# Optimization experiments

Measured on AMD Instinct MI355X. Metric: run time of the kernel, lower is better.

Reference implementation:

```python
import jax, jax.numpy as jnp
import numpy as np

B, IN, OUT, LAT = 8192, 256, 256, 128

def setup_inputs() -> dict:
    key = jax.random.key(0)
    ks = jax.random.split(key, 6)
    s = 0.05
    return {
        "x": jax.random.normal(ks[0], (B, IN), dtype=jnp.float32),
        "latent": jax.random.normal(ks[1], (B, LAT), dtype=jnp.float32),
        "Ww": jax.random.normal(ks[2], (LAT, IN * OUT), dtype=jnp.float32) * s,
        "bw": jax.random.normal(ks[3], (IN * OUT,), dtype=jnp.float32) * s,
        "Wb": jax.random.normal(ks[4], (LAT, OUT), dtype=jnp.float32) * s,
        "bb": jax.random.normal(ks[5], (OUT,), dtype=jnp.float32) * s,
    }

def reference(x, latent, Ww, bw, Wb, bb):
    lead = x.shape[:-1]
    x2 = x.reshape(-1, x.shape[-1])            # [B, in]
    l2 = latent.reshape(-1, latent.shape[-1])  # [B, lat]
    # per-sample weight: [B, in, out]
    weight = (l2 @ Ww + bw).reshape(-1, IN, OUT)
    # per-sample bias: [B, out]
    bias = l2 @ Wb + bb
    out = jnp.einsum('bi,bio->bo', x2, weight) + bias
    return out.reshape(*lead, OUT)
```

## Files before the change

kernel.cpp:

```cpp
#include <hip/hip_runtime.h>
#include <cstdint>
#include <cstddef>

#define BATCH  8192
#define IN_N   256
#define OUT_N  256
#define LAT_N  128
#define SLABS  129
#define KT     (SLABS * IN_N)
#define KT16   (KT / 16)
#define SPLITK 4

typedef _Float16 h8 __attribute__((ext_vector_type(8)));
typedef _Float16 h4 __attribute__((ext_vector_type(4)));
typedef _Float16 h2 __attribute__((ext_vector_type(2)));
typedef float    f16v __attribute__((ext_vector_type(16)));
typedef float    f4v  __attribute__((ext_vector_type(4)));

#define WS_BP    0
#define WS_XH    16908288
#define WS_LT    21102592
#define WS_PARTS 23216128

#define PR_T1   516
#define PR_L1   580
#define PR_X1   1604
#define PR_O1   1608
#define PR_B1   2632
__global__ void k_prep(const float* __restrict__ Ww, const float* __restrict__ bw,
                       const float* __restrict__ x,  const float* __restrict__ latent,
                       const float* __restrict__ Wb, const float* __restrict__ bb,
                       _Float16* __restrict__ Bp, _Float16* __restrict__ Xh,
                       _Float16* __restrict__ LT, float* __restrict__ part0) {
    __shared__ _Float16 smemh[16512];
    const int bid = blockIdx.x;
    const int t   = threadIdx.x;

    if (bid < PR_T1) {
        _Float16* tile = smemh;
        const int k0 = bid * 64;
#pragma unroll
        for (int j = 0; j < 16; ++j) {
            int idx = j * 256 + t;
            int row = idx >> 6, col = (idx & 63) * 4;
            int k = k0 + row;
            const float* src = (k < LAT_N * IN_N)
                             ? Ww + (size_t)k * 256 + col
                             : bw + (size_t)(k - LAT_N * IN_N) * 256 + col;
            float4 v = *(const float4*)src;
            h4 o;
            o[0] = (_Float16)v.x; o[1] = (_Float16)v.y;
            o[2] = (_Float16)v.z; o[3] = (_Float16)v.w;
            *(h4*)(tile + row * 256 + col) = o;
        }
        __syncthreads();
        const int tl = t & 31;
#pragma unroll
        for (int j = 0; j < 4; ++j) {
            int stid = j * 8 + (t >> 5);
            int kt_l = stid >> 3, nt = stid & 7;
            int kt16 = bid * 4 + kt_l;
            _Float16* dst = Bp + ((size_t)(nt * KT16 + kt16) * 64) * 8;
#pragma unroll
            for (int kh = 0; kh < 2; ++kh) {
                h8 v;
#pragma unroll
                for (int h = 0; h < 8; ++h)
                    v[h] = tile[(kt_l * 16 + kh * 8 + h) * 256 + nt * 32 + tl];
                *(h8*)(dst + (size_t)(kh * 32 + tl) * 8) = v;
            }
        }
    } else if (bid < PR_L1) {
        _Float16* t2 = smemh;
        const int b0 = (bid - PR_T1) * 128;
#pragma unroll
        for (int j = 0; j < 16; ++j) {
            int idx = j * 256 + t;
            int b = idx >> 5, l = (idx & 31) * 4;
            float4 v = *(const float4*)(latent + (size_t)(b0 + b) * 128 + l);
            t2[(l + 0) * 129 + b] = (_Float16)v.x;
            t2[(l + 1) * 129 + b] = (_Float16)v.y;
            t2[(l + 2) * 129 + b] = (_Float16)v.z;
            t2[(l + 3) * 129 + b] = (_Float16)v.w;
        }
        __syncthreads();
#pragma unroll
        for (int j = 0; j < 32; ++j) {
            int idx = j * 256 + t;
            int l = idx >> 6, bb = (idx & 63) * 2;
            h2 w;
            w[0] = t2[l * 129 + bb];
            w[1] = t2[l * 129 + bb + 1];
            *(h2*)(LT + (size_t)l * BATCH + b0 + bb) = w;
        }
    } else if (bid < PR_X1) {
        const int cb = bid - PR_L1;
        int i = (cb * 256 + t) * 8;
        float4 v0 = *(const float4*)(x + i);
        float4 v1 = *(const float4*)(x + i + 4);
        h8 o;
        o[0] = (_Float16)v0.x; o[1] = (_Float16)v0.y;
        o[2] = (_Float16)v0.z; o[3] = (_Float16)v0.w;
        o[4] = (_Float16)v1.x; o[5] = (_Float16)v1.y;
        o[6] = (_Float16)v1.z; o[7] = (_Float16)v1.w;
        *(h8*)(Xh + i) = o;
    } else if (bid < PR_O1) {
        const int ob = bid - PR_X1;
        int base = ob * 2048 + t * 8;
        h8 o;
#pragma unroll
        for (int h = 0; h < 8; ++h) o[h] = (_Float16)1.0f;
        *(h8*)(LT + (size_t)LAT_N * BATCH + base) = o;
    } else {
        float* lat = (float*)smemh;
        const int b0 = (bid - PR_O1) * 8;
#pragma unroll
        for (int j = 0; j < 4; ++j) {
            int idx = t + 256 * j;
            int rr = idx >> 7, l = idx & 127;
            lat[rr * 128 + l] = latent[(size_t)(b0 + rr) * 128 + l];
        }
        __syncthreads();
        const int o = t;
        float acc[8];
        float bbv = bb[o];
#pragma unroll
        for (int rr = 0; rr < 8; ++rr) acc[rr] = bbv;
        for (int l = 0; l < 128; ++l) {
            float w = Wb[l * 256 + o];
#pragma unroll
            for (int rr = 0; rr < 8; ++rr) acc[rr] += lat[rr * 128 + l] * w;
        }
#pragma unroll
        for (int rr = 0; rr < 8; ++rr) part0[(size_t)(b0 + rr) * 256 + o] = acc[rr];
    }
}

__global__ __launch_bounds__(256, 2) void k_gemm(const _Float16* __restrict__ Bp,
                                                 const _Float16* __restrict__ Xh,
                                                 const _Float16* __restrict__ LT,
                                                 float* __restrict__ parts) {
    __shared__ _Float16 Xs[64 * 256];

    const int bid   = blockIdx.x;
    const int m_blk = bid >> 2;
    const int ks    = bid & 3;
    const int m0    = m_blk * 64;
    const int slab0 = (ks == 0) ? 0 : 33 + 32 * (ks - 1);
    const int nslab = (ks == 0) ? 33 : 32;

    const int tid = threadIdx.x, wid = tid >> 6, lane = tid & 63;
    const int l32 = lane & 31, khalf = lane >> 5;

    for (int j = 0; j < 8; ++j) {
        int G = j * 256 + tid;
        int m = G >> 5, gp = G & 31;
        int g = gp ^ (m & 7);
        h8 v = *(const h8*)(Xh + (size_t)(m0 + m) * IN_N + g * 8);
        *(h8*)(Xs + m * IN_N + gp * 8) = v;
    }
    __syncthreads();

    int mrow[2], m7[2], pbase[2], m6[2];
#pragma unroll
    for (int t = 0; t < 2; ++t) {
        mrow[t]  = t * 32 + l32;
        m7[t]    = mrow[t] & 7;
        m6[t]    = m7[t] & 6;
        pbase[t] = mrow[t] * IN_N + (khalf ^ (m7[t] & 1)) * 8;
    }

    const _Float16* ltp = LT + (size_t)slab0 * BATCH + m0;
    _Float16 s_cur[2], s_nxt[2];
#pragma unroll
    for (int t = 0; t < 2; ++t) s_cur[t] = ltp[mrow[t]];

    const _Float16* bp0 = Bp + ((size_t)((wid * 2 + 0) * KT16 + slab0 * 16) * 64 + lane) * 8;
    const _Float16* bp1 = Bp + ((size_t)((wid * 2 + 1) * KT16 + slab0 * 16) * 64 + lane) * 8;

    f16v acc[2][2];
#pragma unroll
    for (int t = 0; t < 2; ++t)
#pragma unroll
        for (int u = 0; u < 2; ++u)
#pragma unroll
            for (int r = 0; r < 16; ++r) acc[t][u][r] = 0.0f;

    for (int sl = 0; sl < nslab; ++sl) {
        if (sl) {
#pragma unroll
            for (int t = 0; t < 2; ++t) s_cur[t] = s_nxt[t];
        }
        if (sl + 1 < nslab) {
            const _Float16* p = ltp + (size_t)(sl + 1) * BATCH;
#pragma unroll
            for (int t = 0; t < 2; ++t) s_nxt[t] = p[mrow[t]];
        }
        h8 s8[2];
#pragma unroll
        for (int t = 0; t < 2; ++t) {
            _Float16 s = s_cur[t];
            s8[t][0]=s; s8[t][1]=s; s8[t][2]=s; s8[t][3]=s;
            s8[t][4]=s; s8[t][5]=s; s8[t][6]=s; s8[t][7]=s;
        }
        const _Float16* b0p = bp0 + (size_t)sl * (16 * 512);
        const _Float16* b1p = bp1 + (size_t)sl * (16 * 512);
#pragma unroll
        for (int ks16 = 0; ks16 < 16; ++ks16) {
            h8 b0 = *(const h8*)(b0p + ks16 * 512);
            h8 b1 = *(const h8*)(b1p + ks16 * 512);
            h8 a[2];
#pragma unroll
            for (int t = 0; t < 2; ++t) {
                int off = pbase[t] + ((ks16 * 2) ^ m6[t]) * 8;
                h8 xv = *(const h8*)(Xs + off);
                a[t] = xv * s8[t];
            }
#pragma unroll
            for (int t = 0; t < 2; ++t) {
                acc[t][0] = __builtin_amdgcn_mfma_f32_32x32x16_f16(a[t], b0, acc[t][0], 0, 0, 0);
                acc[t][1] = __builtin_amdgcn_mfma_f32_32x32x16_f16(a[t], b1, acc[t][1], 0, 0, 0);
            }
        }
    }

    float* dst = parts + (size_t)ks * ((size_t)BATCH * OUT_N);
#pragma unroll
    for (int t = 0; t < 2; ++t) {
        int rowb = m0 + t * 32;
#pragma unroll
        for (int u = 0; u < 2; ++u) {
            int col = wid * 64 + u * 32 + l32;
#pragma unroll
            for (int r = 0; r < 16; ++r) {
                int row = rowb + (r & 3) + 8 * (r >> 2) + 4 * khalf;
                size_t off = (size_t)row * OUT_N + col;
                float v = acc[t][u][r];
                if (ks == 0) dst[off] += v;
                else         dst[off] = v;
            }
        }
    }
}

__global__ void k_reduce(const float* __restrict__ parts, float* __restrict__ out) {
    int i = (blockIdx.x * 256 + threadIdx.x) * 4;
    f4v s = *(const f4v*)(parts + i);
    s += *(const f4v*)(parts + 2097152 + i);
    s += *(const f4v*)(parts + 2 * 2097152 + i);
    s += *(const f4v*)(parts + 3 * 2097152 + i);
    *(f4v*)(out + i) = s;
}

extern "C" void kernel_launch(void* const* d_in, const int* in_sizes, int n_in,
                              void* d_out, int out_size, void* d_ws, size_t ws_size,
                              hipStream_t stream) {
    const float* x      = (const float*)d_in[0];
    const float* latent = (const float*)d_in[1];
    const float* Ww     = (const float*)d_in[2];
    const float* bw     = (const float*)d_in[3];
    const float* Wb     = (const float*)d_in[4];
    const float* bb     = (const float*)d_in[5];

    char* ws = (char*)d_ws;
    _Float16* Bp    = (_Float16*)(ws + WS_BP);
    _Float16* Xh    = (_Float16*)(ws + WS_XH);
    _Float16* LT    = (_Float16*)(ws + WS_LT);
    float*    parts = (float*)(ws + WS_PARTS);
    float*    out   = (float*)d_out;

    k_prep<<<PR_B1, 256, 0, stream>>>(Ww, bw, x, latent, Wb, bb, Bp, Xh, LT, parts);
    k_gemm<<<512, 256, 0, stream>>>(Bp, Xh, LT, parts);
    k_reduce<<<2048, 256, 0, stream>>>(parts, out);
}
```

Baseline: 273.1 us.

## Stage B tiles through LDS with async global_load_lds pipeline, keep X in registers

Restructures the GEMM kernel so the large B operand (packed expanded weights) is loaded into a 4-deep LDS ring buffer with direct global-to-LDS async loads and shared by all 8 waves, rather than each wave streaming B from global memory directly. X rows now stay in registers, M tile grows to 128 with 512-thread blocks (grid halved), and each wave computes a 32x128 tile. This cuts redundant global B traffic per output row and overlaps loads with MFMA, at the cost of a barrier per k-step, more register use and fewer blocks for the GPU.

```diff
diff --git a/kernel.cpp b/kernel.cpp
--- a/kernel.cpp
+++ b/kernel.cpp
@@ -16,6 +16,12 @@
 typedef _Float16 h2 __attribute__((ext_vector_type(2)));
 typedef float    f16v __attribute__((ext_vector_type(16)));
 typedef float    f4v  __attribute__((ext_vector_type(4)));
+
+#define AS1 __attribute__((address_space(1)))
+#define AS3 __attribute__((address_space(3)))
+#define WAITVM0 asm volatile("s_waitcnt vmcnt(0)" ::: "memory")
+#define WAITVM2 asm volatile("s_waitcnt vmcnt(2)" ::: "memory")
+#define WAITVM3 asm volatile("s_waitcnt vmcnt(3)" ::: "memory")
 
 #define WS_BP    0
 #define WS_XH    16908288
@@ -87,11 +93,11 @@
 #pragma unroll
         for (int j = 0; j < 32; ++j) {
             int idx = j * 256 + t;
-            int l = idx >> 6, bb = (idx & 63) * 2;
+            int l = idx >> 6, bb2 = (idx & 63) * 2;
             h2 w;
-            w[0] = t2[l * 129 + bb];
-            w[1] = t2[l * 129 + bb + 1];
-            *(h2*)(LT + (size_t)l * BATCH + b0 + bb) = w;
+            w[0] = t2[l * 129 + bb2];
+            w[1] = t2[l * 129 + bb2 + 1];
+            *(h2*)(LT + (size_t)l * BATCH + b0 + bb2) = w;
         }
     } else if (bid < PR_X1) {
         const int cb = bid - PR_L1;
@@ -136,111 +142,125 @@
     }
 }
 
-__global__ __launch_bounds__(256, 2) void k_gemm(const _Float16* __restrict__ Bp,
+__global__ __launch_bounds__(512, 2) void k_gemm(const _Float16* __restrict__ Bp,
                                                  const _Float16* __restrict__ Xh,
                                                  const _Float16* __restrict__ LT,
                                                  float* __restrict__ parts) {
-    __shared__ _Float16 Xs[64 * 256];
+    __shared__ __align__(16) _Float16 Bs[4 * 8192];
 
     const int bid   = blockIdx.x;
+    const int ks    = bid & 3;
     const int m_blk = bid >> 2;
-    const int ks    = bid & 3;
-    const int m0    = m_blk * 64;
+    const int m0    = m_blk * 128;
     const int slab0 = (ks == 0) ? 0 : 33 + 32 * (ks - 1);
     const int nslab = (ks == 0) ? 33 : 32;
 
     const int tid = threadIdx.x, wid = tid >> 6, lane = tid & 63;
     const int l32 = lane & 31, khalf = lane >> 5;
-
-    for (int j = 0; j < 8; ++j) {
-        int G = j * 256 + tid;
-        int m = G >> 5, gp = G & 31;
-        int g = gp ^ (m & 7);
-        h8 v = *(const h8*)(Xh + (size_t)(m0 + m) * IN_N + g * 8);
-        *(h8*)(Xs + m * IN_N + gp * 8) = v;
-    }
-    __syncthreads();
-
-    int mrow[2], m7[2], pbase[2], m6[2];
-#pragma unroll
-    for (int t = 0; t < 2; ++t) {
-        mrow[t]  = t * 32 + l32;
-        m7[t]    = mrow[t] & 7;
-        m6[t]    = m7[t] & 6;
-        pbase[t] = mrow[t] * IN_N + (khalf ^ (m7[t] & 1)) * 8;
-    }
-
-    const _Float16* ltp = LT + (size_t)slab0 * BATCH + m0;
-    _Float16 s_cur[2], s_nxt[2];
-#pragma unroll
-    for (int t = 0; t < 2; ++t) s_cur[t] = ltp[mrow[t]];
-
-    const _Float16* bp0 = Bp + ((size_t)((wid * 2 + 0) * KT16 + slab0 * 16) * 64 + lane) * 8;
-    const _Float16* bp1 = Bp + ((size_t)((wid * 2 + 1) * KT16 + slab0 * 16) * 64 + lane) * 8;
-
-    f16v acc[2][2];
-#pragma unroll
-    for (int t = 0; t < 2; ++t)
-#pragma unroll
-        for (int u = 0; u < 2; ++u)
-#pragma unroll
-            for (int r = 0; r < 16; ++r) acc[t][u][r] = 0.0f;
-
-    for (int sl = 0; sl < nslab; ++sl) {
-        if (sl) {
-#pragma unroll
-            for (int t = 0; t < 2; ++t) s_cur[t] = s_nxt[t];
-        }
-        if (sl + 1 < nslab) {
-            const _Float16* p = ltp + (size_t)(sl + 1) * BATCH;
-#pragma unroll
-            for (int t = 0; t < 2; ++t) s_nxt[t] = p[mrow[t]];
-        }
-        h8 s8[2];
-#pragma unroll
-        for (int t = 0; t < 2; ++t) {
-            _Float16 s = s_cur[t];
-            s8[t][0]=s; s8[t][1]=s; s8[t][2]=s; s8[t][3]=s;
-            s8[t][4]=s; s8[t][5]=s; s8[t][6]=s; s8[t][7]=s;
-        }
-        const _Float16* b0p = bp0 + (size_t)sl * (16 * 512);
-        const _Float16* b1p = bp1 + (size_t)sl * (16 * 512);
-#pragma unroll
-        for (int ks16 = 0; ks16 < 16; ++ks16) {
-            h8 b0 = *(const h8*)(b0p + ks16 * 512);
-            h8 b1 = *(const h8*)(b1p + ks16 * 512);
-            h8 a[2];
-#pragma unroll
-            for (int t = 0; t < 2; ++t) {
-                int off = pbase[t] + ((ks16 * 2) ^ m6[t]) * 8;
-                h8 xv = *(const h8*)(Xs + off);
-                a[t] = xv * s8[t];
+    const int wm = wid >> 1, wn = wid & 1;
+    const int wn4 = wn * 4;
+    const int mrow = m0 + wm * 32 + l32;
+
+    h8 xv[16];
+    const _Float16* xp = Xh + (size_t)mrow * IN_N + khalf * 8;
+#pragma unroll
+    for (int k = 0; k < 16; ++k) xv[k] = *(const h8*)(xp + k * 16);
+
+    const _Float16* ltp = LT + (size_t)slab0 * BATCH;
+    _Float16 s_cur = ltp[mrow];
+
+    const int chunk0 = wid * 2;
+    const int ktl0 = chunk0 >> 3, nt0 = chunk0 & 7;
+    const char* Bgb = (const char*)Bp;
+
+#define STAGE(bufidx, ktg)                                                                 \
+    do {                                                                                   \
+        const char* g0_ = Bgb + (((size_t)(nt0 * KT16 + (ktg) + ktl0)) << 10) + (lane << 4);     \
+        const char* g1_ = Bgb + (((size_t)((nt0 + 1) * KT16 + (ktg) + ktl0)) << 10) + (lane << 4); \
+        _Float16* l0_ = Bs + (bufidx) * 8192 + chunk0 * 512;                               \
+        __builtin_amdgcn_global_load_lds((const AS1 void*)g0_, (AS3 void*)l0_, 16, 0, 0);  \
+        __builtin_amdgcn_global_load_lds((const AS1 void*)g1_, (AS3 void*)(l0_ + 512), 16, 0, 0); \
+    } while (0)
+
+    f16v acc0, acc1, acc2, acc3;
+#pragma unroll
+    for (int r = 0; r < 16; ++r) { acc0[r] = 0.f; acc1[r] = 0.f; acc2[r] = 0.f; acc3[r] = 0.f; }
+
+#define KSTEP(bufc, sl)                                                                    \
+    _Pragma("unroll")                                                                      \
+    for (int j = 0; j < 2; ++j) {                                                          \
+        const int kx = (((sl) * 2 + j) & 15);                                              \
+        h8 a = xv[kx] * s8;                                                                \
+        const _Float16* bb = Bs + (bufc) * 8192 + j * 4096 + wn4 * 512 + (lane << 3);      \
+        h8 b0 = *(const h8*)(bb);                                                          \
+        h8 b1 = *(const h8*)(bb + 512);                                                    \
+        h8 b2 = *(const h8*)(bb + 1024);                                                   \
+        h8 b3 = *(const h8*)(bb + 1536);                                                   \
+        acc0 = __builtin_amdgcn_mfma_f32_32x32x16_f16(a, b0, acc0, 0, 0, 0);               \
+        acc1 = __builtin_amdgcn_mfma_f32_32x32x16_f16(a, b1, acc1, 0, 0, 0);               \
+        acc2 = __builtin_amdgcn_mfma_f32_32x32x16_f16(a, b2, acc2, 0, 0, 0);               \
+        acc3 = __builtin_amdgcn_mfma_f32_32x32x16_f16(a, b3, acc3, 0, 0, 0);               \
+    }
+
+    const int kb = slab0 * 16;
+
+    STAGE(0, kb + 0);
+    STAGE(1, kb + 2);
+    WAITVM2;
+    __builtin_amdgcn_s_barrier();
+    asm volatile("" ::: "memory");
+
+    for (int s0 = 0; s0 < nslab - 1; ++s0) {
+        _Float16 s_nx = ltp[(size_t)(s0 + 1) * BATCH + mrow];
+        h8 s8;
+#pragma unroll
+        for (int h = 0; h < 8; ++h) s8[h] = s_cur;
+        const int ktg0 = kb + s0 * 16;
+#pragma unroll
+        for (int sl = 0; sl < 8; ++sl) {
+            STAGE((sl + 2) & 3, ktg0 + (sl + 2) * 2);
+            KSTEP(sl & 3, sl);
+            if (sl == 0) WAITVM3; else WAITVM2;
+            __builtin_amdgcn_s_barrier();
+            asm volatile("" ::: "memory");
+        }
+        s_cur = s_nx;
+    }
+
+    {
+        h8 s8;
+#pragma unroll
+        for (int h = 0; h < 8; ++h) s8[h] = s_cur;
+        const int ktg0 = kb + (nslab - 1) * 16;
+#pragma unroll
+        for (int sl = 0; sl < 8; ++sl) {
+            if (sl < 6) STAGE((sl + 2) & 3, ktg0 + (sl + 2) * 2);
+            KSTEP(sl & 3, sl);
+            if (sl < 7) {
+                if (sl == 6) WAITVM0; else WAITVM2;
+                __builtin_amdgcn_s_barrier();
+                asm volatile("" ::: "memory");
             }
-#pragma unroll
-            for (int t = 0; t < 2; ++t) {
-                acc[t][0] = __builtin_amdgcn_mfma_f32_32x32x16_f16(a[t], b0, acc[t][0], 0, 0, 0);
-                acc[t][1] = __builtin_amdgcn_mfma_f32_32x32x16_f16(a[t], b1, acc[t][1], 0, 0, 0);
-            }
         }
     }
 
     float* dst = parts + (size_t)ks * ((size_t)BATCH * OUT_N);
-#pragma unroll
-    for (int t = 0; t < 2; ++t) {
-        int rowb = m0 + t * 32;
-#pragma unroll
-        for (int u = 0; u < 2; ++u) {
-            int col = wid * 64 + u * 32 + l32;
-#pragma unroll
-            for (int r = 0; r < 16; ++r) {
-                int row = rowb + (r & 3) + 8 * (r >> 2) + 4 * khalf;
-                size_t off = (size_t)row * OUT_N + col;
-                float v = acc[t][u][r];
-                if (ks == 0) dst[off] += v;
-                else         dst[off] = v;
-            }
-        }
-    }
+    const int rowb = m0 + wm * 32;
+#define EPI(u, accv)                                                                       \
+    {                                                                                      \
+        int col = wn * 128 + (u) * 32 + l32;                                               \
+        _Pragma("unroll")                                                                  \
+        for (int r = 0; r < 16; ++r) {                                                     \
+            int row = rowb + (r & 3) + 8 * (r >> 2) + 4 * khalf;                           \
+            size_t off = (size_t)row * OUT_N + col;                                        \
+            if (ks == 0) dst[off] += accv[r];                                              \
+            else         dst[off] = accv[r];                                               \
+        }                                                                                  \
+    }
+    EPI(0, acc0); EPI(1, acc1); EPI(2, acc2); EPI(3, acc3);
+#undef EPI
+#undef KSTEP
+#undef STAGE
 }
 
 __global__ void k_reduce(const float* __restrict__ parts, float* __restrict__ out) {
@@ -270,6 +290,6 @@
     float*    out   = (float*)d_out;
 
     k_prep<<<PR_B1, 256, 0, stream>>>(Ww, bw, x, latent, Wb, bb, Bp, Xh, LT, parts);
-    k_gemm<<<512, 256, 0, stream>>>(Bp, Xh, LT, parts);
+    k_gemm<<<256, 512, 0, stream>>>(Bp, Xh, LT, parts);
     k_reduce<<<2048, 256, 0, stream>>>(parts, out);
 }
```

After: 252.2 us. 7.7% less time.
